# Performance work log

Measured on AMD Instinct MI355X. Metric: run time of the kernel, lower is better.

The kernel has to match this reference:

```python
import jax, jax.numpy as jnp
import numpy as np
from jax import lax

B, T, N = 8, 64, 512          # batch, seq_len, num_nodes
H, G1, G2 = 128, 128, 64      # lstm_hidden_dim, gcn_hidden, gcn_out
E = 8192                      # num_edges (avg degree 16)


def setup_inputs() -> dict:
    key = jax.random.key(0)
    ks = jax.random.split(key, 20)
    s = 0.05
    inp = {}
    inp["x"] = jax.random.normal(ks[0], (B, T, N), jnp.float32)
    inp["edge_index"] = jax.random.randint(ks[1], (2, E), 0, N, dtype=jnp.int64)
    in_sizes = [1, H, H]
    for l in range(3):
        inp[f"w_ih{l}"] = jax.random.normal(ks[2 + 4 * l], (4 * H, in_sizes[l]), jnp.float32) * s
        inp[f"w_hh{l}"] = jax.random.normal(ks[3 + 4 * l], (4 * H, H), jnp.float32) * s
        inp[f"b_ih{l}"] = jax.random.normal(ks[4 + 4 * l], (4 * H,), jnp.float32) * s
        inp[f"b_hh{l}"] = jax.random.normal(ks[5 + 4 * l], (4 * H,), jnp.float32) * s
    inp["gcn1_w"] = jax.random.normal(ks[14], (G1, H), jnp.float32) * s
    inp["gcn1_b"] = jnp.zeros((G1,), jnp.float32)
    inp["gcn2_w"] = jax.random.normal(ks[15], (G2, G1), jnp.float32) * s
    inp["gcn2_b"] = jnp.zeros((G2,), jnp.float32)
    inp["cls_w"] = jax.random.normal(ks[16], (1, G2), jnp.float32) * s
    inp["cls_b"] = jnp.zeros((1,), jnp.float32)
    return inp


def _lstm_layer(x, w_ih, w_hh, b_ih, b_hh):
    # x: [S, T, D] -> [S, T, H]; PyTorch gate order i, f, g, o.
    S = x.shape[0]
    Hh = w_hh.shape[1]
    # precompute input projections for all timesteps: [T, S, 4H]
    xp = jnp.swapaxes(jnp.einsum('std,gd->stg', x, w_ih) + b_ih + b_hh, 0, 1)

    def step(carry, xt):
        h, c = carry
        gates = xt + h @ w_hh.T
        i, f, g, o = jnp.split(gates, 4, axis=-1)
        c = jax.nn.sigmoid(f) * c + jax.nn.sigmoid(i) * jnp.tanh(g)
        h = jax.nn.sigmoid(o) * jnp.tanh(c)
        return (h, c), h

    init = (jnp.zeros((S, Hh), x.dtype), jnp.zeros((S, Hh), x.dtype))
    _, hs = lax.scan(step, init, xp)
    return jnp.swapaxes(hs, 0, 1)  # [S, T, H]


def reference(x, edge_index, w_ih0, w_hh0, b_ih0, b_hh0,
              w_ih1, w_hh1, b_ih1, b_hh1, w_ih2, w_hh2, b_ih2, b_hh2,
              gcn1_w, gcn1_b, gcn2_w, gcn2_b, cls_w, cls_b):
    Bz, Tt, Nn = x.shape
    # [B, T, N] -> [B*N, T, 1]
    h = jnp.transpose(x, (0, 2, 1)).reshape(Bz * Nn, Tt, 1)
    h = _lstm_layer(h, w_ih0, w_hh0, b_ih0, b_hh0)  # dropout inactive in eval
    h = _lstm_layer(h, w_ih1, w_hh1, b_ih1, b_hh1)
    h = _lstm_layer(h, w_ih2, w_hh2, b_ih2, b_hh2)
    feats = h[:, -1, :].reshape(Bz, Nn, -1)  # [B, N, H]

    # GCNConv: add self-loops, symmetric normalization (PyG default).
    loop = jnp.arange(Nn, dtype=edge_index.dtype)
    src = jnp.concatenate([edge_index[0], loop])
    dst = jnp.concatenate([edge_index[1], loop])
    deg = jnp.zeros((Nn,), feats.dtype).at[dst].add(1.0)
    dis = deg ** -0.5  # deg >= 1 due to self-loops
    norm = dis[src] * dis[dst]  # [E+N]

    def gcn(xn, W, b):
        xl = xn @ W.T                                  # [B, N, out]
        msg = xl[:, src, :] * norm[None, :, None]      # [B, E+N, out]
        agg = jnp.zeros_like(xl).at[:, dst, :].add(msg)
        return agg + b

    h1 = jax.nn.relu(gcn(feats, gcn1_w, gcn1_b))
    h2 = jax.nn.relu(gcn(h1, gcn2_w, gcn2_b))
    pooled = h2.mean(axis=1)                           # global mean pool per graph
    return pooled @ cls_w.T + cls_b                    # [B, 1]
```

## Files before the change

### kernel.cpp

```cpp
#include <hip/hip_runtime.h>

#define TT   64
#define NB   8
#define NN   512
#define HID  128
#define G4   512
#define EE   8192
#define SBLK 16
#define NTHR 512
#define TCH  32
#define NCH  2

#define LOG2E 1.44269504088896f

__device__ __forceinline__ float fsig(float x){
  return __builtin_amdgcn_rcpf(1.0f + __builtin_amdgcn_exp2f(-x*LOG2E));
}
__device__ __forceinline__ float ftanh(float x){
  return 1.0f - 2.0f*__builtin_amdgcn_rcpf(__builtin_amdgcn_exp2f(2.0f*LOG2E*x) + 1.0f);
}

using half8 = __attribute__((ext_vector_type(8))) _Float16;
using f32x4 = __attribute__((ext_vector_type(4))) float;

__device__ __forceinline__ void keepv(half8& v){
  asm volatile("" : "+v"(*(f32x4*)&v));
}

__global__ void prep_w(const float* __restrict__ whh0, const float* __restrict__ wih1,
                       const float* __restrict__ whh1, const float* __restrict__ wih2,
                       const float* __restrict__ whh2, _Float16* __restrict__ wp)
{
  int idx = blockIdx.x*256 + threadIdx.x;
  int mat = idx >> 16;
  int r   = (idx >> 7) & 511;
  int k   = idx & 127;
  const float* src = (mat==0)?whh0:(mat==1)?wih1:(mat==2)?whh1:(mat==3)?wih2:whh2;
  float v = src[r*HID + k];
  int kt = k >> 5, kk = k & 31, s0 = kk >> 3, j = kk & 7;
  int nt = r >> 4, half = nt >> 4, nl = nt & 15;
  int l  = (r & 15) + 16*s0;
  wp[(mat*8 + kt*2 + half)*8192 + nl*512 + l*8 + j] = (_Float16)v;
}

template<int L>
__device__ __forceinline__ void scan_phase(
    int ch, const _Float16* __restrict__ wp, _Float16* __restrict__ hsave,
    _Float16* hseq, _Float16* hb, const _Float16* xall,
    float4 bL, float4 w0g, float (&cs)[4], float (&hlast)[4])
{
  const int tid  = threadIdx.x;
  const int lane = tid & 63, wv = tid >> 6, row = lane & 15;
  const int u    = 16*wv + row;
  const int blk  = blockIdx.x;

  __syncthreads();

  const char* whhG = (const char*)(wp + (L==0?0:(L==1?2:4))*65536);
  half8 Wf[4][4];
  #pragma unroll
  for (int g=0;g<4;g++)
    #pragma unroll
    for (int kt=0;kt<4;kt++){
      Wf[g][kt] = *(const half8*)(whhG + kt*32768 + (g>>1)*16384
                                  + (wv+8*(g&1))*1024 + lane*16);
      keepv(Wf[g][kt]);
    }
  half8 wih[4][4];
  if (L>0){
    const char* wihG = (const char*)(wp + (L==1?1:3)*65536);
    #pragma unroll
    for (int g=0;g<4;g++)
      #pragma unroll
      for (int kt=0;kt<4;kt++){
        wih[g][kt] = *(const half8*)(wihG + kt*32768 + (g>>1)*16384
                                     + (wv+8*(g&1))*1024 + lane*16);
        keepv(wih[g][kt]);
      }
  }

  if (ch == 0){
    for (int i=tid;i<2048;i+=NTHR) hb[i] = (_Float16)0.0f;
  } else {
    const unsigned long long* s =
      (const unsigned long long*)(hsave + (size_t)(L*256+blk)*4096);
    ((unsigned long long*)hb)[tid] = s[tid];
  }

  int rboff[4], wbyteW[4], stoffW[4];
  #pragma unroll
  for (int kt=0;kt<4;kt++)
    rboff[kt] = row*256 + (((kt<<6) + ((lane>>4)<<4)) ^ ((row&7)<<4));
  #pragma unroll
  for (int r=0;r<4;r++){
    int sq = 4*(lane>>4)+r;
    wbyteW[r] = sq*256 + ((u*2) ^ ((sq&7)<<4));
    stoffW[r] = (wv>>1)*512 + (2*(wv&1)+((lane&15)>>3))*128 + sq*8 + (lane&7);
  }

  __syncthreads();

  const char* hseq_c = (const char*)hseq;
  half8 pfA[4];
  if (L>0){
    #pragma unroll
    for (int kt=0;kt<4;kt++)
      pfA[kt] = *(const half8*)(hseq_c + kt*1024 + lane*16);
  }

  #pragma unroll 1
  for (int tt=0; tt<TCH; ++tt){
    const int t = ch*TCH + tt;
    __syncthreads();

    f32x4 acc[4];
    #pragma unroll
    for (int g=0;g<4;g++) acc[g] = (f32x4){bL[g],bL[g],bL[g],bL[g]};

    if (L>0){
      #pragma unroll
      for (int g=0;g<4;g++)
        #pragma unroll
        for (int kt=0;kt<4;kt++)
          acc[g] = __builtin_amdgcn_mfma_f32_16x16x32_f16(pfA[kt], wih[g][kt], acc[g],0,0,0);
    }

    const char* hbR = (const char*)hb + (tt&1)*4096;
    half8 ahh[4];
    #pragma unroll
    for (int kt=0;kt<4;kt++)
      ahh[kt] = *(const half8*)(hbR + rboff[kt]);
    #pragma unroll
    for (int g=0;g<4;g++)
      #pragma unroll
      for (int kt=0;kt<4;kt++)
        acc[g] = __builtin_amdgcn_mfma_f32_16x16x32_f16(ahh[kt], Wf[g][kt], acc[g],0,0,0);

    if (L>0 && tt+1 < TCH){
      #pragma unroll
      for (int kt=0;kt<4;kt++)
        pfA[kt] = *(const half8*)(hseq_c + (tt+1)*4096 + kt*1024 + lane*16);
    }

    char* hbW = (char*)hb + ((tt+1)&1)*4096;
    _Float16* sq16 = hseq + tt*2048;
    #pragma unroll
    for (int r=0;r<4;r++){
      float iv=acc[0][r], fv=acc[1][r], gv=acc[2][r], ov=acc[3][r];
      if (L==0){
        float xv = (float)xall[t*SBLK + 4*(lane>>4)+r];
        iv+=xv*w0g[0]; fv+=xv*w0g[1]; gv+=xv*w0g[2]; ov+=xv*w0g[3];
      }
      float cn = fsig(fv)*cs[r] + fsig(iv)*ftanh(gv);
      cs[r]=cn; float hn = fsig(ov)*ftanh(cn);
      _Float16 hh = (_Float16)hn;
      *(_Float16*)(hbW + wbyteW[r]) = hh;
      if (L<2) sq16[stoffW[r]] = hh;
      if (L==2 && t==TT-1) hlast[r]=hn;
    }
  }

  __syncthreads();
  if (NCH>1 && ch==0){
    unsigned long long* d =
      (unsigned long long*)(hsave + (size_t)(L*256+blk)*4096);
    d[tid] = ((const unsigned long long*)((const char*)hb + (TCH&1)*4096))[tid];
  }
}

__global__ __launch_bounds__(NTHR,2) void lstm_scan(
    const float* __restrict__ x,    const float* __restrict__ wih0,
    const float* __restrict__ bih0, const float* __restrict__ bhh0,
    const float* __restrict__ bih1, const float* __restrict__ bhh1,
    const float* __restrict__ bih2, const float* __restrict__ bhh2,
    const _Float16* __restrict__ wp, _Float16* __restrict__ hsave,
    float* __restrict__ feats)
{
  __shared__ __align__(16) _Float16 hseq[TCH*2048];
  __shared__ __align__(16) _Float16 hb[2*2048];
  __shared__ __align__(16) _Float16 xall[TT*SBLK];

  const int tid  = threadIdx.x;
  const int lane = tid & 63, wv = tid >> 6;
  const int u    = 16*wv + (lane & 15);
  const int s0   = blockIdx.x * SBLK;
  const int b    = s0 >> 9, n0 = s0 & (NN-1);

  for (int i = tid; i < TT*SBLK; i += NTHR)
    xall[i] = (_Float16)x[(b*TT + (i>>4))*NN + n0 + (i&15)];

  float4 b0, b1, b2, w0g;
  #pragma unroll
  for (int g=0; g<4; g++){
    b0[g]  = bih0[g*HID+u] + bhh0[g*HID+u];
    b1[g]  = bih1[g*HID+u] + bhh1[g*HID+u];
    b2[g]  = bih2[g*HID+u] + bhh2[g*HID+u];
    w0g[g] = wih0[g*HID+u];
  }

  float cs0[4]={0,0,0,0}, cs1[4]={0,0,0,0}, cs2[4]={0,0,0,0};
  float hlast[4]={0,0,0,0};

  #pragma unroll 1
  for (int ch=0; ch<NCH; ++ch){
    scan_phase<0>(ch, wp, hsave, hseq, hb, xall, b0, w0g, cs0, hlast);
    scan_phase<1>(ch, wp, hsave, hseq, hb, xall, b1, w0g, cs1, hlast);
    scan_phase<2>(ch, wp, hsave, hseq, hb, xall, b2, w0g, cs2, hlast);
  }

  #pragma unroll
  for (int r=0;r<4;r++)
    feats[(s0 + 4*(lane>>4) + r)*HID + u] = hlast[r];
}

template<int KOUT>
__global__ void gcn_gemm(const float* __restrict__ in, const float* __restrict__ W,
                         const float* __restrict__ pre_bias, float* __restrict__ out)
{
  int id  = blockIdx.x*256 + threadIdx.x;
  int row = id / KOUT;
  int o   = id & (KOUT-1);
  const float4* a4 = (const float4*)(in + row*HID);
  const float4* w4 = (const float4*)(W + o*HID);
  float acc = 0.f;
  if (pre_bias){
    const float4* b4 = (const float4*)pre_bias;
    #pragma unroll 8
    for (int k=0;k<HID/4;k++){
      float4 av=a4[k], wv=w4[k], bv=b4[k];
      acc += fmaxf(av.x+bv.x,0.f)*wv.x + fmaxf(av.y+bv.y,0.f)*wv.y
           + fmaxf(av.z+bv.z,0.f)*wv.z + fmaxf(av.w+bv.w,0.f)*wv.w;
    }
  } else {
    #pragma unroll 8
    for (int k=0;k<HID/4;k++){
      float4 av=a4[k], wv=w4[k];
      acc += av.x*wv.x + av.y*wv.y + av.z*wv.z + av.w*wv.w;
    }
  }
  out[id] = acc;
}

__global__ void deg_init(float* deg){
  int i = blockIdx.x*256 + threadIdx.x;
  if (i < NN) deg[i] = 1.0f;
}
__global__ void deg_edges(const int* __restrict__ ei, float* deg){
  int e = blockIdx.x*256 + threadIdx.x;
  if (e < EE) atomicAdd(&deg[ei[EE+e]], 1.0f);
}
__global__ void build_A(const int* __restrict__ ei, const float* __restrict__ deg,
                        float* __restrict__ A){
  int e = blockIdx.x*256 + threadIdx.x;
  if (e < EE){
    int s = ei[e], d = ei[EE+e];
    atomicAdd(&A[d*NN+s], rsqrtf(deg[s])*rsqrtf(deg[d]));
  } else if (e < EE+NN){
    int n = e - EE;
    atomicAdd(&A[n*NN+n], 1.0f/deg[n]);
  }
}

template<int KOUT>
__global__ __launch_bounds__(512) void gcn_agg(const float* __restrict__ A,
    const float* __restrict__ X, float* __restrict__ Y)
{
  const int F4 = KOUT/4;
  const int TN = 16;
  __shared__ __align__(16) float As[TN*NN];
  const int b = blockIdx.x, n0 = blockIdx.y*TN;
  const int tid = threadIdx.x;
  const int f4 = tid & (F4-1), nr = tid / F4;
  for (int i = tid; i < TN*NN; i += TN*F4) As[i] = A[n0*NN + i];
  __syncthreads();
  const float* Xb = X + b*NN*KOUT + f4*4;
  const float* Ar = As + nr*NN;
  float4 s = {0,0,0,0};
  #pragma unroll 4
  for (int m=0;m<NN;m++){
    float a = Ar[m];
    float4 xv = *(const float4*)(Xb + m*KOUT);
    s.x += a*xv.x; s.y += a*xv.y; s.z += a*xv.z; s.w += a*xv.w;
  }
  *(float4*)(Y + (b*NN + n0 + nr)*KOUT + f4*4) = s;
}

__global__ void finalize(const float* __restrict__ agg2, const float* __restrict__ b2,
                         const float* __restrict__ clw, const float* __restrict__ clb,
                         float* __restrict__ out)
{
  __shared__ float red[256];
  int bb = blockIdx.x, tid = threadIdx.x;
  float acc = 0.f;
  for (int i = tid; i < NN*64; i += 256){
    int j = i & 63;
    float v = agg2[bb*NN*64 + i] + b2[j];
    acc += fmaxf(v, 0.f) * clw[j];
  }
  red[tid] = acc; __syncthreads();
  for (int sfd=128; sfd>0; sfd>>=1){
    if (tid < sfd) red[tid] += red[tid+sfd];
    __syncthreads();
  }
  if (tid==0) out[bb] = red[0]*(1.0f/NN) + clb[0];
}

extern "C" void kernel_launch(void* const* d_in, const int* in_sizes, int n_in,
                              void* d_out, int out_size, void* d_ws, size_t ws_size,
                              hipStream_t stream)
{
  const float* x    = (const float*)d_in[0];
  const int*   ei   = (const int*)  d_in[1];
  const float* wih0 = (const float*)d_in[2];
  const float* whh0 = (const float*)d_in[3];
  const float* bih0 = (const float*)d_in[4];
  const float* bhh0 = (const float*)d_in[5];
  const float* wih1 = (const float*)d_in[6];
  const float* whh1 = (const float*)d_in[7];
  const float* bih1 = (const float*)d_in[8];
  const float* bhh1 = (const float*)d_in[9];
  const float* wih2 = (const float*)d_in[10];
  const float* whh2 = (const float*)d_in[11];
  const float* bih2 = (const float*)d_in[12];
  const float* bhh2 = (const float*)d_in[13];
  const float* g1w  = (const float*)d_in[14];
  const float* g1b  = (const float*)d_in[15];
  const float* g2w  = (const float*)d_in[16];
  const float* g2b  = (const float*)d_in[17];
  const float* clw  = (const float*)d_in[18];
  const float* clb  = (const float*)d_in[19];
  float* out = (float*)d_out;

  char* ws = (char*)d_ws;
  float* feats = (float*)(ws);
  float* xl1   = (float*)(ws + 2097152);
  float* agg1  = (float*)(ws + 4194304);
  float* xl2   = (float*)(ws + 6291456);
  float* agg2  = (float*)(ws + 7340032);
  float* A     = (float*)(ws + 8388608);
  float* deg   = (float*)(ws + 9437184);

  _Float16* hsaveW = (_Float16*)(ws);
  _Float16* wpW    = (_Float16*)(ws + 6291456);

  prep_w<<<(5*G4*HID)/256, 256, 0, stream>>>(whh0, wih1, whh1, wih2, whh2, wpW);

  hipMemsetAsync(A, 0, NN*NN*sizeof(float), stream);
  deg_init <<<2, 256, 0, stream>>>(deg);
  deg_edges<<<EE/256, 256, 0, stream>>>(ei, deg);
  build_A  <<<(EE+NN+255)/256, 256, 0, stream>>>(ei, deg, A);

  lstm_scan<<<256, NTHR, 0, stream>>>(x, wih0, bih0, bhh0,
      bih1, bhh1, bih2, bhh2, wpW, hsaveW, feats);

  gcn_gemm<128><<<(4096*128)/256, 256, 0, stream>>>(feats, g1w, nullptr, xl1);
  gcn_agg<128><<<dim3(NB, NN/16), 512, 0, stream>>>(A, xl1, agg1);
  gcn_gemm<64><<<(4096*64)/256, 256, 0, stream>>>(agg1, g2w, g1b, xl2);
  gcn_agg<64><<<dim3(NB, NN/16), 256, 0, stream>>>(A, xl2, agg2);
  finalize<<<NB, 256, 0, stream>>>(agg2, g2b, clw, clb, out);
}
```

Measured before the change: 574.3 us.

## Split LSTM gate GEMM K dimension across two wave halves with LDS reduction

```diff
diff --git a/kernel.cpp b/kernel.cpp
--- a/kernel.cpp
+++ b/kernel.cpp
@@ -7,9 +7,9 @@
 #define G4   512
 #define EE   8192
 #define SBLK 16
-#define NTHR 512
-#define TCH  32
-#define NCH  2
+#define NTHR 1024
+#define TCH  16
+#define NCH  4
 
 #define LOG2E 1.44269504088896f
 
@@ -45,130 +45,152 @@
 
 template<int L>
 __device__ __forceinline__ void scan_phase(
-    int ch, const _Float16* __restrict__ wp, _Float16* __restrict__ hsave,
-    _Float16* hseq, _Float16* hb, const _Float16* xall,
-    float4 bL, float4 w0g, float (&cs)[4], float (&hlast)[4])
+    int ch, const _Float16* __restrict__ wp,
+    const float* __restrict__ bihL, const float* __restrict__ bhhL,
+    const float* __restrict__ wih0, _Float16* __restrict__ hsave,
+    _Float16* hseq, _Float16* hb, float* exch, const _Float16* xall,
+    float (&cs)[2], float* __restrict__ feats)
 {
   const int tid  = threadIdx.x;
   const int lane = tid & 63, wv = tid >> 6, row = lane & 15;
-  const int u    = 16*wv + row;
+  const int ug   = wv & 7, kh = wv >> 3;
+  const int u    = 16*ug + row;
   const int blk  = blockIdx.x;
+  const int s0b  = blk * SBLK;
 
   __syncthreads();
 
   const char* whhG = (const char*)(wp + (L==0?0:(L==1?2:4))*65536);
-  half8 Wf[4][4];
+  half8 Wf[4][2];
   #pragma unroll
   for (int g=0;g<4;g++)
     #pragma unroll
-    for (int kt=0;kt<4;kt++){
-      Wf[g][kt] = *(const half8*)(whhG + kt*32768 + (g>>1)*16384
-                                  + (wv+8*(g&1))*1024 + lane*16);
-      keepv(Wf[g][kt]);
-    }
-  half8 wih[4][4];
+    for (int j=0;j<2;j++){
+      int nt = g*8 + ug;
+      Wf[g][j] = *(const half8*)(whhG + (2*kh+j)*32768 + (nt>>4)*16384
+                                 + (nt&15)*1024 + lane*16);
+      keepv(Wf[g][j]);
+    }
+  half8 Uf[4][2];
   if (L>0){
     const char* wihG = (const char*)(wp + (L==1?1:3)*65536);
     #pragma unroll
     for (int g=0;g<4;g++)
       #pragma unroll
-      for (int kt=0;kt<4;kt++){
-        wih[g][kt] = *(const half8*)(wihG + kt*32768 + (g>>1)*16384
-                                     + (wv+8*(g&1))*1024 + lane*16);
-        keepv(wih[g][kt]);
+      for (int j=0;j<2;j++){
+        int nt = g*8 + ug;
+        Uf[g][j] = *(const half8*)(wihG + (2*kh+j)*32768 + (nt>>4)*16384
+                                   + (nt&15)*1024 + lane*16);
+        keepv(Uf[g][j]);
       }
+  }
+
+  float bs[4], w0g[4];
+  #pragma unroll
+  for (int g=0;g<4;g++){
+    bs[g] = bihL[g*HID+u] + bhhL[g*HID+u];
+    w0g[g] = (L==0) ? wih0[g*HID+u] : 0.0f;
   }
 
   if (ch == 0){
     for (int i=tid;i<2048;i+=NTHR) hb[i] = (_Float16)0.0f;
   } else {
-    const unsigned long long* s =
-      (const unsigned long long*)(hsave + (size_t)(L*256+blk)*4096);
-    ((unsigned long long*)hb)[tid] = s[tid];
-  }
-
-  int rboff[4], wbyteW[4], stoffW[4];
+    ((unsigned*)hb)[tid] =
+      ((const unsigned*)(hsave + (size_t)(L*256+blk)*4096))[tid];
+  }
+
+  int rboff[2];
   #pragma unroll
-  for (int kt=0;kt<4;kt++)
-    rboff[kt] = row*256 + (((kt<<6) + ((lane>>4)<<4)) ^ ((row&7)<<4));
+  for (int j=0;j<2;j++)
+    rboff[j] = row*256 + ((((2*kh+j)<<6) + ((lane>>4)<<4)) ^ ((row&7)<<4));
+  const int sqa = 4*(lane>>4) + 2*kh, sqb = sqa + 1;
+  const int wbyA = sqa*256 + ((u*2) ^ ((sqa&7)<<4));
+  const int wbyB = sqb*256 + ((u*2) ^ ((sqb&7)<<4));
+  const int stA  = (ug>>1)*512 + (2*(ug&1)+(row>>3))*128 + sqa*8 + (lane&7);
+  const int stB  = stA + 8;
+  int exWr[4], exRd[4];
   #pragma unroll
-  for (int r=0;r<4;r++){
-    int sq = 4*(lane>>4)+r;
-    wbyteW[r] = sq*256 + ((u*2) ^ ((sq&7)<<4));
-    stoffW[r] = (wv>>1)*512 + (2*(wv&1)+((lane&15)>>3))*128 + sq*8 + (lane&7);
+  for (int g=0;g<4;g++){
+    exWr[g] = ((kh*32     + ug*4 + g)*64 + lane)*4;
+    exRd[g] = (((1-kh)*32 + ug*4 + g)*64 + lane)*4;
   }
 
   __syncthreads();
-
-  const char* hseq_c = (const char*)hseq;
-  half8 pfA[4];
-  if (L>0){
-    #pragma unroll
-    for (int kt=0;kt<4;kt++)
-      pfA[kt] = *(const half8*)(hseq_c + kt*1024 + lane*16);
-  }
 
   #pragma unroll 1
   for (int tt=0; tt<TCH; ++tt){
     const int t = ch*TCH + tt;
+
+    const char* hbR = (const char*)hb + (tt&1)*4096;
+    half8 ahh0 = *(const half8*)(hbR + rboff[0]);
+    half8 ahh1 = *(const half8*)(hbR + rboff[1]);
+    f32x4 acc[4];
+    #pragma unroll
+    for (int g=0;g<4;g++) acc[g] = (f32x4){0.f,0.f,0.f,0.f};
+    if (L>0){
+      const char* hs = (const char*)hseq + tt*4096;
+      half8 p0 = *(const half8*)(hs + (2*kh+0)*1024 + lane*16);
+      half8 p1 = *(const half8*)(hs + (2*kh+1)*1024 + lane*16);
+      #pragma unroll
+      for (int g=0;g<4;g++){
+        acc[g] = __builtin_amdgcn_mfma_f32_16x16x32_f16(p0, Uf[g][0], acc[g],0,0,0);
+        acc[g] = __builtin_amdgcn_mfma_f32_16x16x32_f16(p1, Uf[g][1], acc[g],0,0,0);
+      }
+    }
+    #pragma unroll
+    for (int g=0;g<4;g++){
+      acc[g] = __builtin_amdgcn_mfma_f32_16x16x32_f16(ahh0, Wf[g][0], acc[g],0,0,0);
+      acc[g] = __builtin_amdgcn_mfma_f32_16x16x32_f16(ahh1, Wf[g][1], acc[g],0,0,0);
+    }
+    #pragma unroll
+    for (int g=0;g<4;g++) *(f32x4*)(exch + exWr[g]) = acc[g];
+
     __syncthreads();
 
-    f32x4 acc[4];
-    #pragma unroll
-    for (int g=0;g<4;g++) acc[g] = (f32x4){bL[g],bL[g],bL[g],bL[g]};
-
-    if (L>0){
-      #pragma unroll
-      for (int g=0;g<4;g++)
-        #pragma unroll
-        for (int kt=0;kt<4;kt++)
-          acc[g] = __builtin_amdgcn_mfma_f32_16x16x32_f16(pfA[kt], wih[g][kt], acc[g],0,0,0);
-    }
-
-    const char* hbR = (const char*)hb + (tt&1)*4096;
-    half8 ahh[4];
-    #pragma unroll
-    for (int kt=0;kt<4;kt++)
-      ahh[kt] = *(const half8*)(hbR + rboff[kt]);
-    #pragma unroll
-    for (int g=0;g<4;g++)
-      #pragma unroll
-      for (int kt=0;kt<4;kt++)
-        acc[g] = __builtin_amdgcn_mfma_f32_16x16x32_f16(ahh[kt], Wf[g][kt], acc[g],0,0,0);
-
-    if (L>0 && tt+1 < TCH){
-      #pragma unroll
-      for (int kt=0;kt<4;kt++)
-        pfA[kt] = *(const half8*)(hseq_c + (tt+1)*4096 + kt*1024 + lane*16);
+    float ga[4], gb[4];
+    #pragma unroll
+    for (int g=0;g<4;g++){
+      f32x4 og = *(const f32x4*)(exch + exRd[g]);
+      float v0 = acc[g][0]+og[0], v1 = acc[g][1]+og[1];
+      float v2 = acc[g][2]+og[2], v3 = acc[g][3]+og[3];
+      ga[g] = bs[g] + (kh ? v2 : v0);
+      gb[g] = bs[g] + (kh ? v3 : v1);
     }
 
     char* hbW = (char*)hb + ((tt+1)&1)*4096;
     _Float16* sq16 = hseq + tt*2048;
-    #pragma unroll
-    for (int r=0;r<4;r++){
-      float iv=acc[0][r], fv=acc[1][r], gv=acc[2][r], ov=acc[3][r];
-      if (L==0){
-        float xv = (float)xall[t*SBLK + 4*(lane>>4)+r];
-        iv+=xv*w0g[0]; fv+=xv*w0g[1]; gv+=xv*w0g[2]; ov+=xv*w0g[3];
-      }
-      float cn = fsig(fv)*cs[r] + fsig(iv)*ftanh(gv);
-      cs[r]=cn; float hn = fsig(ov)*ftanh(cn);
+    {
+      float iv=ga[0], fv=ga[1], gv=ga[2], ov=ga[3];
+      if (L==0){ float xv = (float)xall[t*SBLK + sqa];
+                 iv+=xv*w0g[0]; fv+=xv*w0g[1]; gv+=xv*w0g[2]; ov+=xv*w0g[3]; }
+      float cn = fsig(fv)*cs[0] + fsig(iv)*ftanh(gv);
+      cs[0]=cn; float hn = fsig(ov)*ftanh(cn);
       _Float16 hh = (_Float16)hn;
-      *(_Float16*)(hbW + wbyteW[r]) = hh;
-      if (L<2) sq16[stoffW[r]] = hh;
-      if (L==2 && t==TT-1) hlast[r]=hn;
-    }
-  }
-
-  __syncthreads();
-  if (NCH>1 && ch==0){
-    unsigned long long* d =
-      (unsigned long long*)(hsave + (size_t)(L*256+blk)*4096);
-    d[tid] = ((const unsigned long long*)((const char*)hb + (TCH&1)*4096))[tid];
-  }
-}
-
-__global__ __launch_bounds__(NTHR,2) void lstm_scan(
+      *(_Float16*)(hbW + wbyA) = hh;
+      if (L<2) sq16[stA] = hh;
+      if (L==2 && t==TT-1) feats[(s0b + sqa)*HID + u] = hn;
+    }
+    {
+      float iv=gb[0], fv=gb[1], gv=gb[2], ov=gb[3];
+      if (L==0){ float xv = (float)xall[t*SBLK + sqb];
+                 iv+=xv*w0g[0]; fv+=xv*w0g[1]; gv+=xv*w0g[2]; ov+=xv*w0g[3]; }
+      float cn = fsig(fv)*cs[1] + fsig(iv)*ftanh(gv);
+      cs[1]=cn; float hn = fsig(ov)*ftanh(cn);
+      _Float16 hh = (_Float16)hn;
+      *(_Float16*)(hbW + wbyB) = hh;
+      if (L<2) sq16[stB] = hh;
+      if (L==2 && t==TT-1) feats[(s0b + sqb)*HID + u] = hn;
+    }
+
+    __syncthreads();
+  }
+
+  if (ch < NCH-1){
+    ((unsigned*)(hsave + (size_t)(L*256+blk)*4096))[tid] = ((const unsigned*)hb)[tid];
+  }
+}
+
+__global__ __launch_bounds__(NTHR,1) void lstm_scan(
     const float* __restrict__ x,    const float* __restrict__ wih0,
     const float* __restrict__ bih0, const float* __restrict__ bhh0,
     const float* __restrict__ bih1, const float* __restrict__ bhh1,
@@ -177,40 +199,25 @@
     float* __restrict__ feats)
 {
   __shared__ __align__(16) _Float16 hseq[TCH*2048];
+  __shared__ __align__(16) float    exch[16384];
   __shared__ __align__(16) _Float16 hb[2*2048];
   __shared__ __align__(16) _Float16 xall[TT*SBLK];
 
-  const int tid  = threadIdx.x;
-  const int lane = tid & 63, wv = tid >> 6;
-  const int u    = 16*wv + (lane & 15);
-  const int s0   = blockIdx.x * SBLK;
-  const int b    = s0 >> 9, n0 = s0 & (NN-1);
-
-  for (int i = tid; i < TT*SBLK; i += NTHR)
-    xall[i] = (_Float16)x[(b*TT + (i>>4))*NN + n0 + (i&15)];
-
-  float4 b0, b1, b2, w0g;
-  #pragma unroll
-  for (int g=0; g<4; g++){
-    b0[g]  = bih0[g*HID+u] + bhh0[g*HID+u];
-    b1[g]  = bih1[g*HID+u] + bhh1[g*HID+u];
-    b2[g]  = bih2[g*HID+u] + bhh2[g*HID+u];
-    w0g[g] = wih0[g*HID+u];
-  }
-
-  float cs0[4]={0,0,0,0}, cs1[4]={0,0,0,0}, cs2[4]={0,0,0,0};
-  float hlast[4]={0,0,0,0};
+  const int tid = threadIdx.x;
+  const int s0  = blockIdx.x * SBLK;
+  const int b   = s0 >> 9, n0 = s0 & (NN-1);
+
+  if (tid < TT*SBLK)
+    xall[tid] = (_Float16)x[(b*TT + (tid>>4))*NN + n0 + (tid&15)];
+
+  float cs0[2]={0,0}, cs1[2]={0,0}, cs2[2]={0,0};
 
   #pragma unroll 1
   for (int ch=0; ch<NCH; ++ch){
-    scan_phase<0>(ch, wp, hsave, hseq, hb, xall, b0, w0g, cs0, hlast);
-    scan_phase<1>(ch, wp, hsave, hseq, hb, xall, b1, w0g, cs1, hlast);
-    scan_phase<2>(ch, wp, hsave, hseq, hb, xall, b2, w0g, cs2, hlast);
-  }
-
-  #pragma unroll
-  for (int r=0;r<4;r++)
-    feats[(s0 + 4*(lane>>4) + r)*HID + u] = hlast[r];
+    scan_phase<0>(ch, wp, bih0, bhh0, wih0, hsave, hseq, hb, exch, xall, cs0, feats);
+    scan_phase<1>(ch, wp, bih1, bhh1, wih0, hsave, hseq, hb, exch, xall, cs1, feats);
+    scan_phase<2>(ch, wp, bih2, bhh2, wih0, hsave, hseq, hb, exch, xall, cs2, feats);
+  }
 }
 
 template<int KOUT>
```

New measurement: 687.4 us. 19.7% more time.
